# Kernel optimization log

Hardware: AMD Instinct MI355X
Metric: run time of the kernel (lower is better)

## Reference

```python
import jax, jax.numpy as jnp
import numpy as np

NB, B, T, D, H = 7, 16, 512, 128, 2
HD = D // H

def _ln(x, s, b):
    m = jnp.mean(x, -1, keepdims=True)
    v = jnp.mean((x - m) ** 2, -1, keepdims=True)
    return (x - m) * jax.lax.rsqrt(v + 1e-5) * s + b

def setup_inputs():
    key = jax.random.key(0)
    keys = iter(jax.random.split(key, 80))
    def w(*shape):
        return jax.random.normal(next(keys), shape, jnp.float32) * 0.02
    inp = {}
    inp['bands'] = jax.random.normal(next(keys), (NB, B, T, D), jnp.float32)
    for nm in ['Wq', 'Wk', 'Wv', 'Wo']:
        inp[nm] = w(NB, D, D)
    for nm in ['bq', 'bk', 'bv', 'bo']:
        inp[nm] = jnp.zeros((NB, D), jnp.float32)
    inp['g_ls'] = jnp.ones((3, D), jnp.float32); inp['g_lb'] = jnp.zeros((3, D), jnp.float32)
    inp['g_w1'] = w(3, D, 2 * D); inp['g_b1'] = jnp.zeros((3, 2 * D), jnp.float32)
    inp['g_w2'] = w(3, 2 * D, D); inp['g_b2'] = jnp.zeros((3, D), jnp.float32)
    inp['g_wg'] = w(3, D, D);     inp['g_bg'] = jnp.zeros((3, D), jnp.float32)
    inp['h_ls'] = jnp.ones((2, D), jnp.float32); inp['h_lb'] = jnp.zeros((2, D), jnp.float32)
    inp['h_w1'] = w(2, D, 3 * D); inp['h_b1'] = jnp.zeros((2, 3 * D), jnp.float32)
    inp['h_w2'] = w(2, 3 * D, D); inp['h_b2'] = jnp.zeros((2, D), jnp.float32)
    inp['r_ls'] = jnp.ones((2, D), jnp.float32); inp['r_lb'] = jnp.zeros((2, D), jnp.float32)
    inp['r_w1'] = w(2, D, 4 * D); inp['r_b1'] = jnp.zeros((2, 4 * D), jnp.float32)
    inp['r_w2'] = w(2, 4 * D, D); inp['r_b2'] = jnp.zeros((2, D), jnp.float32)
    # wormhole: pairs (0,6),(1,5),(2,4) share cross_proj per pair; bridge on band 3
    inp['wp_w'] = w(3, D, D);     inp['wp_b'] = jnp.zeros((3, D), jnp.float32)
    inp['wg_w'] = w(3, 2 * D, D); inp['wg_b'] = jnp.zeros((3, D), jnp.float32)
    inp['br_w'] = w(6, D, D);     inp['br_b'] = jnp.zeros((6, D), jnp.float32)
    inp['bg_w'] = w(2 * D, D);    inp['bg_b'] = jnp.zeros((D,), jnp.float32)
    return inp

def reference(bands, Wq, bq, Wk, bk, Wv, bv, Wo, bo,
              g_ls, g_lb, g_w1, g_b1, g_w2, g_b2, g_wg, g_bg,
              h_ls, h_lb, h_w1, h_b1, h_w2, h_b2,
              r_ls, r_lb, r_w1, r_b1, r_w2, r_b2,
              wp_w, wp_b, wg_w, wg_b, br_w, br_b, bg_w, bg_b):
    n, b, t, d = bands.shape
    # --- per-band causal self-attention, vectorized over the 7 bands ---
    def heads(x):  # [n,b,t,d] -> [n,b,H,t,hd]
        return x.reshape(n, b, t, H, HD).transpose(0, 1, 3, 2, 4)
    q = heads(jnp.einsum('nbtd,nde->nbte', bands, Wq) + bq[:, None, None, :])
    k = heads(jnp.einsum('nbtd,nde->nbte', bands, Wk) + bk[:, None, None, :])
    v = heads(jnp.einsum('nbtd,nde->nbte', bands, Wv) + bv[:, None, None, :])
    scores = jnp.einsum('nbhtd,nbhsd->nbhts', q, k) / np.float32(np.sqrt(HD))
    causal = jnp.triu(jnp.ones((t, t), bool), 1)
    scores = jnp.where(causal, jnp.float32(-1e9), scores)
    attn = jax.nn.softmax(scores, axis=-1)
    o = jnp.einsum('nbhts,nbhsd->nbhtd', attn, v)
    o = o.transpose(0, 1, 3, 2, 4).reshape(n, b, t, d)
    o = jnp.einsum('nbtd,nde->nbte', o, Wo) + bo[:, None, None, :]
    x = bands + o
    # --- band-tier FFN processors ---
    geo, hyb, rea = x[0:3], x[3:5], x[5:7]
    hg = _ln(geo, g_ls[:, None, None, :], g_lb[:, None, None, :])
    hg = jax.nn.gelu(jnp.einsum('nbtd,nde->nbte', hg, g_w1) + g_b1[:, None, None, :], approximate=False)
    hg = jnp.einsum('nbte,ned->nbtd', hg, g_w2) + g_b2[:, None, None, :]
    gate = jax.nn.sigmoid(jnp.einsum('nbtd,nde->nbte', geo, g_wg) + g_bg[:, None, None, :])
    geo = geo + gate * hg
    hh = _ln(hyb, h_ls[:, None, None, :], h_lb[:, None, None, :])
    hh = jax.nn.gelu(jnp.einsum('nbtd,nde->nbte', hh, h_w1) + h_b1[:, None, None, :], approximate=False)
    hyb = hyb + jnp.einsum('nbte,ned->nbtd', hh, h_w2) + h_b2[:, None, None, :]
    hr = _ln(rea, r_ls[:, None, None, :], r_lb[:, None, None, :])
    hr = jax.nn.gelu(jnp.einsum('nbtd,nde->nbte', hr, r_w1) + r_b1[:, None, None, :], approximate=False)
    rea = rea + jnp.einsum('nbte,ned->nbtd', hr, r_w2) + r_b2[:, None, None, :]
    y = jnp.concatenate([geo, hyb, rea], axis=0)
    # --- position-wise wormhole: pairs (0,6),(1,5),(2,4) + bridge band 3 ---
    bl = y[jnp.array([0, 1, 2])]   # low bands of each pair
    bh = y[jnp.array([6, 5, 4])]   # matching high bands
    info_lo = jnp.einsum('nbtd,nde->nbte', bh, wp_w) + wp_b[:, None, None, :]
    info_hi = jnp.einsum('nbtd,nde->nbte', bl, wp_w) + wp_b[:, None, None, :]
    gate_lo = jax.nn.sigmoid(jnp.einsum('nbtd,nde->nbte', jnp.concatenate([bl, info_lo], -1), wg_w) + wg_b[:, None, None, :])
    gate_hi = jax.nn.sigmoid(jnp.einsum('nbtd,nde->nbte', jnp.concatenate([bh, info_hi], -1), wg_w) + wg_b[:, None, None, :])
    out_lo = bl + gate_lo * info_lo
    out_hi = bh + gate_hi * info_hi
    others = y[jnp.array([0, 1, 2, 4, 5, 6])]
    bridge_info = (jnp.einsum('nbtd,nde->bte', others, br_w) + jnp.sum(br_b, 0)) / 6.0
    gate_br = jax.nn.sigmoid(jnp.concatenate([y[3], bridge_info], -1) @ bg_w + bg_b)
    out3 = y[3] + gate_br * bridge_info
    return jnp.stack([out_lo[0], out_lo[1], out_lo[2], out3, out_hi[2], out_hi[1], out_hi[0]], axis=0)
```

## Files before the change

kernel.cpp:

```cpp
#include <hip/hip_runtime.h>
#include <hip/hip_bf16.h>

#define NBAND 7
#define BBATCH 16
#define TSEQ 512
#define DMODEL 128
#define MBAND (BBATCH * TSEQ)
#define BANDE ((size_t)MBAND * DMODEL)

typedef __attribute__((ext_vector_type(8))) short short8;
typedef __attribute__((ext_vector_type(4))) float f32x4;
typedef unsigned int u32;
typedef unsigned short u16;

__device__ __forceinline__ u16 f2bf(float x) {
  unsigned u = __float_as_uint(x);
  unsigned r = u + 0x7FFF + ((u >> 16) & 1);
  return (u16)(r >> 16);
}
__device__ __forceinline__ u32 pack2(float a, float b) {
  return (u32)f2bf(a) | ((u32)f2bf(b) << 16);
}
__device__ __forceinline__ float b2f(u16 h) {
  return __uint_as_float((u32)h << 16);
}

struct TSlice { const float* src; u16* dst; int K, N; };
struct TArgs { TSlice s[62]; };

__global__ __launch_bounds__(256) void wtrans_kernel(TArgs a) {
  TSlice sl = a.s[blockIdx.z];
  const int tk = (blockIdx.x & 7) * 64, tn = (blockIdx.x >> 3) * 64;
  if (tk >= sl.K || tn >= sl.N) return;
  __shared__ __align__(16) u16 T[64][72];
  const int tid = threadIdx.x;
  #pragma unroll
  for (int it = 0; it < 4; ++it) {
    int idx = tid + it * 256;
    int k = idx >> 4, nq = (idx & 15) << 2;
    float4 v = *(const float4*)&sl.src[(size_t)(tk + k) * sl.N + tn + nq];
    T[nq + 0][k] = f2bf(v.x); T[nq + 1][k] = f2bf(v.y);
    T[nq + 2][k] = f2bf(v.z); T[nq + 3][k] = f2bf(v.w);
  }
  __syncthreads();
  #pragma unroll
  for (int it = 0; it < 2; ++it) {
    int idx = tid + it * 256;
    int n = idx >> 3, kq = (idx & 7) << 3;
    *(short8*)&sl.dst[(size_t)(tn + n) * sl.K + tk + kq] = *(const short8*)&T[n][kq];
  }
}

__device__ __forceinline__ void mfma_part_h(const u16* __restrict__ A,
                                            const u16* __restrict__ WT,
                                            int K, int m0, int n0, int tid,
                                            u16 (*As)[40], u16 (*Bs)[40],
                                            f32x4 acc[2][2]) {
  const int lane = tid & 63;
  const int wv = tid >> 6;
  const int wr = wv >> 1, wc = wv & 1;
  const int lr = lane & 15, k8 = lane >> 4;
  const int row = tid >> 2, kq = (tid & 3) << 3;

  const u16* Ar = &A[(size_t)(m0 + row) * K + kq];
  const u16* Br = &WT[(size_t)(n0 + row) * K + kq];
  short8 apre = *(const short8*)Ar;
  short8 bpre = *(const short8*)Br;

  for (int k0 = 0; k0 < K; k0 += 32) {
    __syncthreads();
    *(short8*)&As[row][kq] = apre;
    *(short8*)&Bs[row][kq] = bpre;
    if (k0 + 32 < K) {
      apre = *(const short8*)(Ar + k0 + 32);
      bpre = *(const short8*)(Br + k0 + 32);
    }
    __syncthreads();
    short8 a0 = *(const short8*)&As[wr * 32 + lr][k8 * 8];
    short8 a1 = *(const short8*)&As[wr * 32 + 16 + lr][k8 * 8];
    short8 b0 = *(const short8*)&Bs[wc * 32 + lr][k8 * 8];
    short8 b1 = *(const short8*)&Bs[wc * 32 + 16 + lr][k8 * 8];
    acc[0][0] = __builtin_amdgcn_mfma_f32_16x16x32_bf16(a0, b0, acc[0][0], 0, 0, 0);
    acc[0][1] = __builtin_amdgcn_mfma_f32_16x16x32_bf16(a0, b1, acc[0][1], 0, 0, 0);
    acc[1][0] = __builtin_amdgcn_mfma_f32_16x16x32_bf16(a1, b0, acc[1][0], 0, 0, 0);
    acc[1][1] = __builtin_amdgcn_mfma_f32_16x16x32_bf16(a1, b1, acc[1][1], 0, 0, 0);
  }
}

struct ZD {
  const u16 *A, *A2, *WT, *WT2;
  const float* bias;
  const float* residF;
  const u16 *residH, *extraH;
  float* OF;
  u16* OH;
  int K, N, op;
  int pad;
};
struct PArgs { ZD z[21]; };

__global__ __launch_bounds__(256) void gemm_b(PArgs p) {
  const ZD d = p.z[blockIdx.z];
  const int n0 = blockIdx.y * 64;
  if (n0 >= d.N) return;
  __shared__ __align__(16) u16 As[64][40];
  __shared__ __align__(16) u16 Bs[64][40];
  const int m0 = blockIdx.x * 64;
  const int tid = threadIdx.x;
  f32x4 acc[2][2] = {};

  mfma_part_h(d.A, d.WT, d.K, m0, n0, tid, As, Bs, acc);
  if (d.A2)
    mfma_part_h(d.A2, d.WT2, d.K, m0, n0, tid, As, Bs, acc);

  const int lane = tid & 63;
  const int wv = tid >> 6;
  const int wr = wv >> 1, wc = wv & 1;
  const int lr = lane & 15, lg = lane >> 4;

  #pragma unroll
  for (int i = 0; i < 2; ++i) {
    #pragma unroll
    for (int j = 0; j < 2; ++j) {
      #pragma unroll
      for (int r = 0; r < 4; ++r) {
        int m = m0 + wr * 32 + i * 16 + lg * 4 + r;
        int n = n0 + wc * 32 + j * 16 + lr;
        float v = acc[i][j][r];
        if (d.bias) v += d.bias[n];
        size_t idx = (size_t)m * d.N + n;
        switch (d.op) {
          case 0: d.OH[idx] = f2bf(v); break;
          case 1: d.OH[idx] =
                    f2bf(0.5f * v * (1.f + erff(v * 0.70710678118654752f))); break;
          case 2: d.OH[idx] = f2bf(1.f / (1.f + __expf(-v))); break;
          case 3: d.OH[idx] = f2bf(d.residF[idx] + v); break;
          case 4: {
            float gate = 1.f / (1.f + __expf(-v));
            d.OF[idx] = b2f(d.residH[idx]) + gate * b2f(d.extraH[idx]);
          } break;
          case 5: {
            float gm = d.extraH ? b2f(d.extraH[idx]) : 1.f;
            d.OH[idx] = f2bf(b2f(d.residH[idx]) + gm * v);
          } break;
          case 6: d.OH[(size_t)n * MBAND + m] = f2bf(v); break;
        }
      }
    }
  }
}

__global__ __launch_bounds__(256) void bridge_kernel(const u16* __restrict__ yb,
                                                     const u16* __restrict__ wtBr,
                                                     const float* __restrict__ br_b,
                                                     u16* __restrict__ O) {
  __shared__ __align__(16) u16 As[64][40];
  __shared__ __align__(16) u16 Bs[64][40];
  const int m0 = blockIdx.x * 64, n0 = blockIdx.y * 64;
  const int tid = threadIdx.x;
  f32x4 acc[2][2] = {};
  const int bl[6] = {0, 1, 2, 4, 5, 6};
  for (int s = 0; s < 6; ++s)
    mfma_part_h(yb + (size_t)bl[s] * BANDE, wtBr + (size_t)s * 16384,
                128, m0, n0, tid, As, Bs, acc);

  const int lane = tid & 63;
  const int wv = tid >> 6;
  const int wr = wv >> 1, wc = wv & 1;
  const int lr = lane & 15, lg = lane >> 4;
  #pragma unroll
  for (int i = 0; i < 2; ++i)
    #pragma unroll
    for (int j = 0; j < 2; ++j) {
      int n = n0 + wc * 32 + j * 16 + lr;
      float bb = 0.f;
      #pragma unroll
      for (int s = 0; s < 6; ++s) bb += br_b[s * 128 + n];
      bb *= (1.f / 6.f);
      #pragma unroll
      for (int r = 0; r < 4; ++r) {
        int m = m0 + wr * 32 + i * 16 + lg * 4 + r;
        O[(size_t)m * 128 + n] = f2bf(acc[i][j][r] * (1.f / 6.f) + bb);
      }
    }
}

__global__ __launch_bounds__(256) void attn_kernel(const u16* __restrict__ q,
                                                   const u16* __restrict__ k,
                                                   const u16* __restrict__ vT,
                                                   u16* __restrict__ o) {
  const int band = blockIdx.x >> 8;
  const int rest = blockIdx.x & 255;
  const int qt = 7 - (rest & 7);
  const int bh = rest >> 3;
  const int h  = bh & 1;
  const int b  = bh >> 1;
  const size_t rowbase = ((size_t)band * BBATCH + b) * TSEQ;
  const u16* vb = vT + (size_t)band * BANDE + (size_t)h * 64 * MBAND + (size_t)b * TSEQ;

  const int tid  = threadIdx.x;
  const int w    = tid >> 6;
  const int lane = tid & 63;
  const int lr   = lane & 15;
  const int lg   = lane >> 4;

  __shared__ __align__(16) u16 Ks[64][72];
  __shared__ __align__(16) u16 Vs[64][72];
  __shared__ __align__(16) u16 Ps[4][16][72];

  short8 aq[2];
  {
    const u16* qp = &q[(rowbase + qt * 64 + w * 16 + lr) * DMODEL + h * 64 + lg * 8];
    aq[0] = *(const short8*)qp;
    aq[1] = *(const short8*)(qp + 32);
  }

  short8 kpre[2], vpre[2];
  #pragma unroll
  for (int it = 0; it < 2; ++it) {
    int idx = tid + it * 256;
    int r = idx >> 3, c8 = (idx & 7) << 3;
    kpre[it] = *(const short8*)&k[(rowbase + r) * DMODEL + h * 64 + c8];
    vpre[it] = *(const short8*)&vb[(size_t)r * MBAND + c8];
  }

  f32x4 oacc[4] = {};
  float m[4], l[4];
  #pragma unroll
  for (int r = 0; r < 4; ++r) { m[r] = -1e30f; l[r] = 0.f; }

  for (int kt = 0; kt <= qt; ++kt) {
    __syncthreads();
    #pragma unroll
    for (int it = 0; it < 2; ++it) {
      int idx = tid + it * 256;
      int r = idx >> 3, c8 = (idx & 7) << 3;
      *(short8*)&Ks[r][c8] = kpre[it];
      *(short8*)&Vs[r][c8] = vpre[it];
    }
    if (kt < qt) {
      int nt = kt + 1;
      #pragma unroll
      for (int it = 0; it < 2; ++it) {
        int idx = tid + it * 256;
        int r = idx >> 3, c8 = (idx & 7) << 3;
        kpre[it] = *(const short8*)&k[(rowbase + nt * 64 + r) * DMODEL + h * 64 + c8];
        vpre[it] = *(const short8*)&vb[(size_t)r * MBAND + nt * 64 + c8];
      }
    }
    __syncthreads();

    f32x4 s[4] = {};
    #pragma unroll
    for (int c = 0; c < 2; ++c) {
      short8 a = aq[c];
      #pragma unroll
      for (int j = 0; j < 4; ++j) {
        short8 bb = *(const short8*)&Ks[j * 16 + lr][c * 32 + lg * 8];
        s[j] = __builtin_amdgcn_mfma_f32_16x16x32_bf16(a, bb, s[j], 0, 0, 0);
      }
    }
    #pragma unroll
    for (int j = 0; j < 4; ++j)
      #pragma unroll
      for (int r = 0; r < 4; ++r)
        s[j][r] *= 0.125f;

    if (kt == qt) {
      #pragma unroll
      for (int j = 0; j < 4; ++j)
        #pragma unroll
        for (int r = 0; r < 4; ++r) {
          int row = w * 16 + lg * 4 + r;
          int col = j * 16 + lr;
          if (col > row) s[j][r] = -1e30f;
        }
    }

    float mx[4], al[4];
    #pragma unroll
    for (int r = 0; r < 4; ++r)
      mx[r] = fmaxf(fmaxf(s[0][r], s[1][r]), fmaxf(s[2][r], s[3][r]));
    #pragma unroll
    for (int off = 1; off <= 8; off <<= 1)
      #pragma unroll
      for (int r = 0; r < 4; ++r)
        mx[r] = fmaxf(mx[r], __shfl_xor(mx[r], off));
    #pragma unroll
    for (int r = 0; r < 4; ++r) {
      float mn = fmaxf(m[r], mx[r]);
      al[r] = __expf(m[r] - mn);
      m[r] = mn;
    }
    float rs[4] = {0.f, 0.f, 0.f, 0.f};
    #pragma unroll
    for (int j = 0; j < 4; ++j)
      #pragma unroll
      for (int r = 0; r < 4; ++r) {
        float pe = __expf(s[j][r] - m[r]);
        s[j][r] = pe;
        rs[r] += pe;
      }
    #pragma unroll
    for (int off = 1; off <= 8; off <<= 1)
      #pragma unroll
      for (int r = 0; r < 4; ++r)
        rs[r] += __shfl_xor(rs[r], off);
    #pragma unroll
    for (int r = 0; r < 4; ++r) l[r] = l[r] * al[r] + rs[r];

    #pragma unroll
    for (int j = 0; j < 4; ++j)
      #pragma unroll
      for (int r = 0; r < 4; ++r)
        oacc[j][r] *= al[r];

    #pragma unroll
    for (int j = 0; j < 4; ++j)
      #pragma unroll
      for (int r = 0; r < 4; ++r)
        Ps[w][lg * 4 + r][j * 16 + lr] = f2bf(s[j][r]);

    #pragma unroll
    for (int c = 0; c < 2; ++c) {
      short8 a = *(const short8*)&Ps[w][lr][c * 32 + lg * 8];
      #pragma unroll
      for (int j = 0; j < 4; ++j) {
        short8 bb = *(const short8*)&Vs[j * 16 + lr][c * 32 + lg * 8];
        oacc[j] = __builtin_amdgcn_mfma_f32_16x16x32_bf16(a, bb, oacc[j], 0, 0, 0);
      }
    }
  }

  float inv[4];
  #pragma unroll
  for (int r = 0; r < 4; ++r) inv[r] = 1.f / l[r];
  #pragma unroll
  for (int j = 0; j < 4; ++j)
    #pragma unroll
    for (int r = 0; r < 4; ++r) {
      size_t row = rowbase + qt * 64 + w * 16 + lg * 4 + r;
      o[row * DMODEL + h * 64 + j * 16 + lr] = f2bf(oacc[j][r] * inv[r]);
    }
}

struct LNA {
  const u16* x;
  u16* xn;
  const float* ls[7];
  const float* lb[7];
};

__global__ __launch_bounds__(256) void ln_kernel(LNA p) {
  const int tid = threadIdx.x;
  const int rr = tid >> 6, lane = tid & 63;
  const size_t row = (size_t)blockIdx.x * 4 + rr;
  u32 wv = *(const u32*)&p.x[row * DMODEL + 2 * lane];
  float a = b2f((u16)wv), b = b2f((u16)(wv >> 16));
  float s = a + b;
  #pragma unroll
  for (int off = 32; off; off >>= 1) s += __shfl_xor(s, off);
  float mean = s * (1.f / 128.f);
  float da = a - mean, db = b - mean;
  float vs = da * da + db * db;
  #pragma unroll
  for (int off = 32; off; off >>= 1) vs += __shfl_xor(vs, off);
  float rstd = rsqrtf(vs * (1.f / 128.f) + 1e-5f);
  int band = (int)(row >> 13);
  const float* ls = p.ls[band];
  const float* lb = p.lb[band];
  *(u32*)&p.xn[row * DMODEL + 2 * lane] =
      pack2(da * rstd * ls[2 * lane] + lb[2 * lane],
            db * rstd * ls[2 * lane + 1] + lb[2 * lane + 1]);
}

__global__ __launch_bounds__(256) void cvt_kernel(const float* __restrict__ in,
                                                  u16* __restrict__ out) {
  size_t i = ((size_t)blockIdx.x * 256 + threadIdx.x) * 8;
  float4 a = *(const float4*)&in[i];
  float4 b = *(const float4*)&in[i + 4];
  uint4 st = {pack2(a.x, a.y), pack2(a.z, a.w), pack2(b.x, b.y), pack2(b.z, b.w)};
  *(uint4*)&out[i] = st;
}

extern "C" void kernel_launch(void* const* d_in, const int* in_sizes, int n_in,
                              void* d_out, int out_size, void* d_ws, size_t ws_size,
                              hipStream_t stream) {
  bool dict = (in_sizes[2] != 896);
  const float* bands = (const float*)d_in[0];
  const float* Wq = (const float*)d_in[1];
  const float *Wk, *Wv, *Wo, *bq, *bk, *bv, *bo;
  if (dict) {
    Wk = (const float*)d_in[2]; Wv = (const float*)d_in[3]; Wo = (const float*)d_in[4];
    bq = (const float*)d_in[5]; bk = (const float*)d_in[6];
    bv = (const float*)d_in[7]; bo = (const float*)d_in[8];
  } else {
    bq = (const float*)d_in[2]; Wk = (const float*)d_in[3]; bk = (const float*)d_in[4];
    Wv = (const float*)d_in[5]; bv = (const float*)d_in[6];
    Wo = (const float*)d_in[7]; bo = (const float*)d_in[8];
  }
  const float* g_ls = (const float*)d_in[9];
  const float* g_lb = (const float*)d_in[10];
  const float* g_w1 = (const float*)d_in[11];
  const float* g_b1 = (const float*)d_in[12];
  const float* g_w2 = (const float*)d_in[13];
  const float* g_b2 = (const float*)d_in[14];
  const float* g_wg = (const float*)d_in[15];
  const float* g_bg = (const float*)d_in[16];
  const float* h_ls = (const float*)d_in[17];
  const float* h_lb = (const float*)d_in[18];
  const float* h_w1 = (const float*)d_in[19];
  const float* h_b1 = (const float*)d_in[20];
  const float* h_w2 = (const float*)d_in[21];
  const float* h_b2 = (const float*)d_in[22];
  const float* r_ls = (const float*)d_in[23];
  const float* r_lb = (const float*)d_in[24];
  const float* r_w1 = (const float*)d_in[25];
  const float* r_b1 = (const float*)d_in[26];
  const float* r_w2 = (const float*)d_in[27];
  const float* r_b2 = (const float*)d_in[28];
  const float* wp_w = (const float*)d_in[29];
  const float* wp_b = (const float*)d_in[30];
  const float* wg_w = (const float*)d_in[31];
  const float* wg_b = (const float*)d_in[32];
  const float* br_w = (const float*)d_in[33];
  const float* br_b = (const float*)d_in[34];
  const float* bg_w = (const float*)d_in[35];
  const float* bg_b = (const float*)d_in[36];
  float* out = (float*)d_out;

  const float* lsP[7] = {g_ls, g_ls + 128, g_ls + 256, h_ls, h_ls + 128, r_ls, r_ls + 128};
  const float* lbP[7] = {g_lb, g_lb + 128, g_lb + 256, h_lb, h_lb + 128, r_lb, r_lb + 128};
  const float* b1p[7] = {g_b1, g_b1 + 256, g_b1 + 512,
                         h_b1, h_b1 + 384, r_b1, r_b1 + 512};
  const float* b2p[7] = {g_b2, g_b2 + 128, g_b2 + 256,
                         h_b2, h_b2 + 128, r_b2, r_b2 + 128};
  const int hN[7] = {256, 256, 256, 384, 384, 512, 512};

  const size_t HIDSZ = (size_t)MBAND * 2560;
  u16* H = (u16*)d_ws;
  u16* hidh   = H;
  u16* bandsH = hidh;
  u16* qh = H + HIDSZ;
  u16* kh = qh + 7 * BANDE;
  u16* vh = kh + 7 * BANDE;
  u16* oh = vh + 7 * BANDE;
  u16* wt = oh + 7 * BANDE;
  u16* wtQ   = wt;
  u16* wtK   = wtQ + 7 * 16384;
  u16* wtV   = wtK + 7 * 16384;
  u16* wtO   = wtV + 7 * 16384;
  u16* wtGwg = wtO + 7 * 16384;
  u16* wtWp  = wtGwg + 3 * 16384;
  u16* wtBr  = wtWp + 3 * 16384;
  u16* wtWg  = wtBr + 6 * 16384;
  u16* wtBg  = wtWg + 6 * 16384;
  u16* wtG1  = wtBg + 2 * 16384;
  u16* wtH1  = wtG1 + 3 * 32768;
  u16* wtR1  = wtH1 + 2 * 49152;
  u16* wtG2  = wtR1 + 2 * 65536;
  u16* wtH2  = wtG2 + 3 * 32768;
  u16* wtR2  = wtH2 + 2 * 49152;
  u16* xh = qh;
  u16* xnh = kh;
  u16* gateh = vh;
  u16* yh = oh;
  u16* infoh = hidh;
  u16* bridgeh = hidh + 6 * BANDE;

  size_t hOff[7];
  {
    size_t acc = 0;
    for (int n = 0; n < 7; ++n) { hOff[n] = acc; acc += (size_t)MBAND * hN[n]; }
  }
  u16* wtW1s[7] = {wtG1, wtG1 + 32768, wtG1 + 65536,
                   wtH1, wtH1 + 49152, wtR1, wtR1 + 65536};
  u16* wtW2s[7] = {wtG2, wtG2 + 32768, wtG2 + 65536,
                   wtH2, wtH2 + 49152, wtR2, wtR2 + 65536};

  auto LP = [&](PArgs& p, int Z, int ymax) {
    dim3 grid(MBAND / 64, ymax, Z);
    gemm_b<<<grid, dim3(256), 0, stream>>>(p);
  };

  cvt_kernel<<<dim3((unsigned)(7 * BANDE / (8 * 256))), dim3(256), 0, stream>>>(bands, bandsH);

  {
    TArgs ta{};
    int ns = 0;
    auto add = [&](const float* s, u16* d, int K, int N) {
      ta.s[ns].src = s; ta.s[ns].dst = d; ta.s[ns].K = K; ta.s[ns].N = N; ++ns;
    };
    for (int z = 0; z < 7; ++z) add(Wq + z * 16384, wtQ + z * 16384, 128, 128);
    for (int z = 0; z < 7; ++z) add(Wk + z * 16384, wtK + z * 16384, 128, 128);
    for (int z = 0; z < 7; ++z) add(Wv + z * 16384, wtV + z * 16384, 128, 128);
    for (int z = 0; z < 7; ++z) add(Wo + z * 16384, wtO + z * 16384, 128, 128);
    for (int i = 0; i < 3; ++i) add(g_wg + i * 16384, wtGwg + i * 16384, 128, 128);
    for (int i = 0; i < 3; ++i) add(wp_w + i * 16384, wtWp + i * 16384, 128, 128);
    for (int j = 0; j < 6; ++j) add(br_w + j * 16384, wtBr + j * 16384, 128, 128);
    for (int i = 0; i < 3; ++i) {
      add(wg_w + i * 32768,         wtWg + (size_t)(2 * i) * 16384,     128, 128);
      add(wg_w + i * 32768 + 16384, wtWg + (size_t)(2 * i + 1) * 16384, 128, 128);
    }
    add(bg_w,         wtBg,         128, 128);
    add(bg_w + 16384, wtBg + 16384, 128, 128);
    for (int i = 0; i < 3; ++i) add(g_w1 + i * 32768, wtG1 + i * 32768, 128, 256);
    for (int i = 0; i < 2; ++i) add(h_w1 + i * 49152, wtH1 + i * 49152, 128, 384);
    for (int i = 0; i < 2; ++i) add(r_w1 + i * 65536, wtR1 + i * 65536, 128, 512);
    for (int i = 0; i < 3; ++i) add(g_w2 + i * 32768, wtG2 + i * 32768, 256, 128);
    for (int i = 0; i < 2; ++i) add(h_w2 + i * 49152, wtH2 + i * 49152, 384, 128);
    for (int i = 0; i < 2; ++i) add(r_w2 + i * 65536, wtR2 + i * 65536, 512, 128);
    wtrans_kernel<<<dim3(64, 1, 62), dim3(256), 0, stream>>>(ta);
  }

  {
    PArgs p{};
    const u16* wtQKV[3] = {wtQ, wtK, wtV};
    const float* bqkv[3] = {bq, bk, bv};
    u16* oqkv[3] = {qh, kh, vh};
    for (int w = 0; w < 3; ++w)
      for (int band = 0; band < 7; ++band) {
        ZD& d = p.z[w * 7 + band];
        d.A = bandsH + (size_t)band * BANDE;
        d.WT = wtQKV[w] + (size_t)band * 16384;
        d.bias = bqkv[w] + band * 128;
        d.OH = oqkv[w] + (size_t)band * BANDE;
        d.K = 128; d.N = 128; d.op = (w == 2) ? 6 : 0;
      }
    LP(p, 21, 2);
  }

  attn_kernel<<<dim3(NBAND * 256), dim3(256), 0, stream>>>(qh, kh, vh, oh);

  {
    PArgs p{};
    for (int band = 0; band < 7; ++band) {
      ZD& d = p.z[band];
      d.A = oh + (size_t)band * BANDE;
      d.WT = wtO + (size_t)band * 16384;
      d.bias = bo + band * 128;
      d.residF = bands + (size_t)band * BANDE;
      d.OH = xh + (size_t)band * BANDE;
      d.K = 128; d.N = 128; d.op = 3;
    }
    LP(p, 7, 2);
  }

  {
    LNA p{};
    p.x = xh; p.xn = xnh;
    for (int n = 0; n < 7; ++n) { p.ls[n] = lsP[n]; p.lb[n] = lbP[n]; }
    ln_kernel<<<dim3(NBAND * MBAND / 4), dim3(256), 0, stream>>>(p);
  }

  {
    PArgs p{};
    for (int z = 0; z < 3; ++z) {
      ZD& d = p.z[z];
      d.A = xh + (size_t)z * BANDE;
      d.WT = wtGwg + (size_t)z * 16384;
      d.bias = g_bg + z * 128;
      d.OH = gateh + (size_t)z * BANDE;
      d.K = 128; d.N = 128; d.op = 2;
    }
    for (int band = 0; band < 7; ++band) {
      ZD& d = p.z[3 + band];
      d.A = xnh + (size_t)band * BANDE;
      d.WT = wtW1s[band];
      d.bias = b1p[band];
      d.OH = hidh + hOff[band];
      d.K = 128; d.N = hN[band]; d.op = 1;
    }
    LP(p, 10, 8);
  }

  {
    PArgs p{};
    for (int band = 0; band < 7; ++band) {
      ZD& d = p.z[band];
      d.A = hidh + hOff[band];
      d.WT = wtW2s[band];
      d.bias = b2p[band];
      d.residH = xh + (size_t)band * BANDE;
      d.extraH = (band < 3) ? gateh + (size_t)band * BANDE : nullptr;
      d.OH = yh + (size_t)band * BANDE;
      d.K = hN[band]; d.N = 128; d.op = 5;
    }
    LP(p, 7, 2);
  }

  {
    PArgs p{};
    for (int z = 0; z < 6; ++z) {
      int t = (z < 3) ? z : z + 1;
      int src = 6 - t;
      int i = (t < 3) ? t : 6 - t;
      ZD& d = p.z[z];
      d.A = yh + (size_t)src * BANDE;
      d.WT = wtWp + (size_t)i * 16384;
      d.bias = wp_b + i * 128;
      d.OH = infoh + (size_t)z * BANDE;
      d.K = 128; d.N = 128; d.op = 0;
    }
    LP(p, 6, 2);
  }

  bridge_kernel<<<dim3(MBAND / 64, 2), dim3(256), 0, stream>>>(yh, wtBr, br_b, bridgeh);

  {
    PArgs p{};
    for (int z = 0; z < 6; ++z) {
      int t = (z < 3) ? z : z + 1;
      int i = (t < 3) ? t : 6 - t;
      ZD& d = p.z[z];
      d.A = yh + (size_t)t * BANDE;
      d.WT = wtWg + (size_t)(2 * i) * 16384;
      d.A2 = infoh + (size_t)z * BANDE;
      d.WT2 = wtWg + (size_t)(2 * i + 1) * 16384;
      d.bias = wg_b + i * 128;
      d.residH = yh + (size_t)t * BANDE;
      d.extraH = infoh + (size_t)z * BANDE;
      d.OF = out + (size_t)t * BANDE;
      d.K = 128; d.N = 128; d.op = 4;
    }
    {
      ZD& d = p.z[6];
      d.A = yh + 3 * BANDE;
      d.WT = wtBg;
      d.A2 = bridgeh;
      d.WT2 = wtBg + 16384;
      d.bias = bg_b;
      d.residH = yh + 3 * BANDE;
      d.extraH = bridgeh;
      d.OF = out + 3 * BANDE;
      d.K = 128; d.N = 128; d.op = 4;
    }
    LP(p, 7, 2);
  }
}
```

Measured before the change: 233.4 us.

## Fuse fp32-to-bf16 conversion into QKV GEMM and merge bridge into wormhole launch

Removes the separate cvt_kernel pass that converted the fp32 bands to bf16; the QKV GEMM now loads fp32 tiles directly and packs them to bf16 while staging into shared memory. The bridge GEMM is folded into the same batched gemm_b launch as the wormhole info projections as a new op 7, saving one kernel launch and letting both run concurrently. In exchange, the QKV GEMM reads the fp32 input three times (once per Q/K/V) instead of the bf16 copy, and gemm_b gains extra branching for the new op.

```diff
diff --git a/kernel.cpp b/kernel.cpp
--- a/kernel.cpp
+++ b/kernel.cpp
@@ -87,8 +87,50 @@
   }
 }
 
+__device__ __forceinline__ void mfma_part_f(const float* __restrict__ A,
+                                            const u16* __restrict__ WT,
+                                            int K, int m0, int n0, int tid,
+                                            u16 (*As)[40], u16 (*Bs)[40],
+                                            f32x4 acc[2][2]) {
+  const int lane = tid & 63;
+  const int wv = tid >> 6;
+  const int wr = wv >> 1, wc = wv & 1;
+  const int lr = lane & 15, k8 = lane >> 4;
+  const int row = tid >> 2, kq = (tid & 3) << 3;
+
+  const float* Ar = &A[(size_t)(m0 + row) * K + kq];
+  const u16* Br = &WT[(size_t)(n0 + row) * K + kq];
+  float4 ap0 = *(const float4*)Ar;
+  float4 ap1 = *(const float4*)(Ar + 4);
+  short8 bpre = *(const short8*)Br;
+
+  for (int k0 = 0; k0 < K; k0 += 32) {
+    __syncthreads();
+    *(u32*)&As[row][kq]     = pack2(ap0.x, ap0.y);
+    *(u32*)&As[row][kq + 2] = pack2(ap0.z, ap0.w);
+    *(u32*)&As[row][kq + 4] = pack2(ap1.x, ap1.y);
+    *(u32*)&As[row][kq + 6] = pack2(ap1.z, ap1.w);
+    *(short8*)&Bs[row][kq] = bpre;
+    if (k0 + 32 < K) {
+      ap0 = *(const float4*)(Ar + k0 + 32);
+      ap1 = *(const float4*)(Ar + k0 + 36);
+      bpre = *(const short8*)(Br + k0 + 32);
+    }
+    __syncthreads();
+    short8 a0 = *(const short8*)&As[wr * 32 + lr][k8 * 8];
+    short8 a1 = *(const short8*)&As[wr * 32 + 16 + lr][k8 * 8];
+    short8 b0 = *(const short8*)&Bs[wc * 32 + lr][k8 * 8];
+    short8 b1 = *(const short8*)&Bs[wc * 32 + 16 + lr][k8 * 8];
+    acc[0][0] = __builtin_amdgcn_mfma_f32_16x16x32_bf16(a0, b0, acc[0][0], 0, 0, 0);
+    acc[0][1] = __builtin_amdgcn_mfma_f32_16x16x32_bf16(a0, b1, acc[0][1], 0, 0, 0);
+    acc[1][0] = __builtin_amdgcn_mfma_f32_16x16x32_bf16(a1, b0, acc[1][0], 0, 0, 0);
+    acc[1][1] = __builtin_amdgcn_mfma_f32_16x16x32_bf16(a1, b1, acc[1][1], 0, 0, 0);
+  }
+}
+
 struct ZD {
   const u16 *A, *A2, *WT, *WT2;
+  const float* AF;
   const float* bias;
   const float* residF;
   const u16 *residH, *extraH;
@@ -109,9 +151,18 @@
   const int tid = threadIdx.x;
   f32x4 acc[2][2] = {};
 
-  mfma_part_h(d.A, d.WT, d.K, m0, n0, tid, As, Bs, acc);
-  if (d.A2)
-    mfma_part_h(d.A2, d.WT2, d.K, m0, n0, tid, As, Bs, acc);
+  if (d.op == 7) {
+    const int bl[6] = {0, 1, 2, 4, 5, 6};
+    #pragma unroll 1
+    for (int s = 0; s < 6; ++s)
+      mfma_part_h(d.A + (size_t)bl[s] * BANDE, d.WT + (size_t)s * 16384,
+                  128, m0, n0, tid, As, Bs, acc);
+  } else {
+    if (d.AF) mfma_part_f(d.AF, d.WT, d.K, m0, n0, tid, As, Bs, acc);
+    else      mfma_part_h(d.A,  d.WT, d.K, m0, n0, tid, As, Bs, acc);
+    if (d.A2)
+      mfma_part_h(d.A2, d.WT2, d.K, m0, n0, tid, As, Bs, acc);
+  }
 
   const int lane = tid & 63;
   const int wv = tid >> 6;
@@ -127,7 +178,7 @@
         int m = m0 + wr * 32 + i * 16 + lg * 4 + r;
         int n = n0 + wc * 32 + j * 16 + lr;
         float v = acc[i][j][r];
-        if (d.bias) v += d.bias[n];
+        if (d.bias && d.op != 7) v += d.bias[n];
         size_t idx = (size_t)m * d.N + n;
         switch (d.op) {
           case 0: d.OH[idx] = f2bf(v); break;
@@ -144,45 +195,16 @@
             d.OH[idx] = f2bf(b2f(d.residH[idx]) + gm * v);
           } break;
           case 6: d.OH[(size_t)n * MBAND + m] = f2bf(v); break;
+          case 7: {
+            float bb = 0.f;
+            #pragma unroll
+            for (int s = 0; s < 6; ++s) bb += d.bias[s * 128 + n];
+            d.OH[idx] = f2bf(v * (1.f / 6.f) + bb * (1.f / 6.f));
+          } break;
         }
       }
     }
   }
-}
-
-__global__ __launch_bounds__(256) void bridge_kernel(const u16* __restrict__ yb,
-                                                     const u16* __restrict__ wtBr,
-                                                     const float* __restrict__ br_b,
-                                                     u16* __restrict__ O) {
-  __shared__ __align__(16) u16 As[64][40];
-  __shared__ __align__(16) u16 Bs[64][40];
-  const int m0 = blockIdx.x * 64, n0 = blockIdx.y * 64;
-  const int tid = threadIdx.x;
-  f32x4 acc[2][2] = {};
-  const int bl[6] = {0, 1, 2, 4, 5, 6};
-  for (int s = 0; s < 6; ++s)
-    mfma_part_h(yb + (size_t)bl[s] * BANDE, wtBr + (size_t)s * 16384,
-                128, m0, n0, tid, As, Bs, acc);
-
-  const int lane = tid & 63;
-  const int wv = tid >> 6;
-  const int wr = wv >> 1, wc = wv & 1;
-  const int lr = lane & 15, lg = lane >> 4;
-  #pragma unroll
-  for (int i = 0; i < 2; ++i)
-    #pragma unroll
-    for (int j = 0; j < 2; ++j) {
-      int n = n0 + wc * 32 + j * 16 + lr;
-      float bb = 0.f;
-      #pragma unroll
-      for (int s = 0; s < 6; ++s) bb += br_b[s * 128 + n];
-      bb *= (1.f / 6.f);
-      #pragma unroll
-      for (int r = 0; r < 4; ++r) {
-        int m = m0 + wr * 32 + i * 16 + lg * 4 + r;
-        O[(size_t)m * 128 + n] = f2bf(acc[i][j][r] * (1.f / 6.f) + bb);
-      }
-    }
 }
 
 __global__ __launch_bounds__(256) void attn_kernel(const u16* __restrict__ q,
@@ -372,15 +394,6 @@
   *(u32*)&p.xn[row * DMODEL + 2 * lane] =
       pack2(da * rstd * ls[2 * lane] + lb[2 * lane],
             db * rstd * ls[2 * lane + 1] + lb[2 * lane + 1]);
-}
-
-__global__ __launch_bounds__(256) void cvt_kernel(const float* __restrict__ in,
-                                                  u16* __restrict__ out) {
-  size_t i = ((size_t)blockIdx.x * 256 + threadIdx.x) * 8;
-  float4 a = *(const float4*)&in[i];
-  float4 b = *(const float4*)&in[i + 4];
-  uint4 st = {pack2(a.x, a.y), pack2(a.z, a.w), pack2(b.x, b.y), pack2(b.z, b.w)};
-  *(uint4*)&out[i] = st;
 }
 
 extern "C" void kernel_launch(void* const* d_in, const int* in_sizes, int n_in,
@@ -439,8 +452,7 @@
 
   const size_t HIDSZ = (size_t)MBAND * 2560;
   u16* H = (u16*)d_ws;
-  u16* hidh   = H;
-  u16* bandsH = hidh;
+  u16* hidh = H;
   u16* qh = H + HIDSZ;
   u16* kh = qh + 7 * BANDE;
   u16* vh = kh + 7 * BANDE;
@@ -483,8 +495,6 @@
     gemm_b<<<grid, dim3(256), 0, stream>>>(p);
   };
 
-  cvt_kernel<<<dim3((unsigned)(7 * BANDE / (8 * 256))), dim3(256), 0, stream>>>(bands, bandsH);
-
   {
     TArgs ta{};
     int ns = 0;
@@ -521,7 +531,7 @@
     for (int w = 0; w < 3; ++w)
       for (int band = 0; band < 7; ++band) {
         ZD& d = p.z[w * 7 + band];
-        d.A = bandsH + (size_t)band * BANDE;
+        d.AF = bands + (size_t)band * BANDE;
         d.WT = wtQKV[w] + (size_t)band * 16384;
         d.bias = bqkv[w] + band * 128;
         d.OH = oqkv[w] + (size_t)band * BANDE;
@@ -602,10 +612,16 @@
       d.OH = infoh + (size_t)z * BANDE;
       d.K = 128; d.N = 128; d.op = 0;
     }
-    LP(p, 6, 2);
-  }
-
-  bridge_kernel<<<dim3(MBAND / 64, 2), dim3(256), 0, stream>>>(yh, wtBr, br_b, bridgeh);
+    {
+      ZD& d = p.z[6];
+      d.A = yh;
+      d.WT = wtBr;
+      d.bias = br_b;
+      d.OH = bridgeh;
+      d.K = 128; d.N = 128; d.op = 7;
+    }
+    LP(p, 7, 2);
+  }
 
   {
     PArgs p{};
```

Result: no change. 231.3 us (-0.9%).
